# Kernel tuning notes

Measured on AMD Instinct MI355X. Metric: run time of the kernel, lower is better.

## Reference

```python
import jax, jax.numpy as jnp
import numpy as np

B, S, D, H = 4, 1024, 1024, 16
DK = D // H


def _linear_params(key, scale):
    kw, kb = jax.random.split(key)
    W = jax.random.normal(kw, (D, D), dtype=jnp.float32) * scale
    b = jax.random.normal(kb, (D,), dtype=jnp.float32) * 0.01
    return W, b


def setup_inputs() -> dict:
    key = jax.random.key(0)
    ks = jax.random.split(key, 12)
    scale = 1.0 / np.sqrt(D)
    inp = {
        "query": jax.random.normal(ks[0], (B, S, D), dtype=jnp.float32),
        "key": jax.random.normal(ks[1], (B, S, D), dtype=jnp.float32),
        "value": jax.random.normal(ks[2], (B, S, D), dtype=jnp.float32),
        "time_k": jax.random.normal(ks[3], (B, S, D), dtype=jnp.float32),
        "time_v": jax.random.normal(ks[4], (B, S, D), dtype=jnp.float32),
        "mask": jnp.zeros((B, 1, S, S), dtype=jnp.float32),
    }
    names = ["Wq", "bq", "Wk", "bk", "Wv", "bv", "Wtk", "btk", "Wtv", "btv", "Wm", "bm"]
    for i in range(6):
        W, b = _linear_params(ks[5 + i], scale)
        inp[names[2 * i]] = W
        inp[names[2 * i + 1]] = b
    return inp


def _split_heads(x):
    # [B,S,D] -> [B,H,S,DK]
    b, s, _ = x.shape
    return x.reshape(b, s, H, DK).transpose(0, 2, 1, 3)


def reference(query, key, value, time_k, time_v, mask,
              Wq, bq, Wk, bk, Wv, bv, Wtk, btk, Wtv, btv, Wm, bm):
    q = _split_heads(query @ Wq + bq)
    k = _split_heads(key @ Wk + bk)
    v = _split_heads(value @ Wv + bv)
    t_k = _split_heads(time_k @ Wtk + btk)
    t_v = _split_heads(time_v @ Wtv + btv)

    # scores[b,h,i,j] = q_i . k_j + t_k_i . q_j  (note second term uses q on the key axis)
    scores = jnp.einsum("bhid,bhjd->bhij", q, k) + jnp.einsum("bhid,bhjd->bhij", t_k, q)
    # module divides by sqrt(d_model) (query.size(-1)), not sqrt(d_k)
    scores = scores / jnp.sqrt(jnp.float32(D)) + mask
    probs = jax.nn.softmax(scores, axis=-1)

    # dropout is identity (p=0 / eval); squeeze(-2) is a no-op for S>1
    context = jnp.einsum("bhij,bhjd->bhid", probs, v) + jnp.einsum("bhij,bhjd->bhid", probs, t_v)
    x = context.transpose(0, 2, 1, 3).reshape(query.shape[0], -1, D)
    return x @ Wm + bm
```

## Files before the change

### kernel.cpp

```cpp
#include <hip/hip_runtime.h>
#include <hip/hip_bf16.h>
#include <cstdint>
#include <cstddef>

typedef __bf16 bf16;
typedef bf16 bf16x8 __attribute__((ext_vector_type(8)));
typedef bf16 bf16x4 __attribute__((ext_vector_type(4)));
typedef float f32x4 __attribute__((ext_vector_type(4)));
typedef unsigned int u32;

#define DEV static __device__ __forceinline__

DEV f32x4 mfma16(bf16x8 a, bf16x8 b, f32x4 c) {
    return __builtin_amdgcn_mfma_f32_16x16x32_bf16(a, b, c, 0, 0, 0);
}

DEV f32x4 shflx4(f32x4 v, int m) {
    f32x4 r;
    for (int i = 0; i < 4; ++i) r[i] = __shfl_xor(v[i], m, 64);
    return r;
}

DEV bf16x8 cvt8(const float* p) {
    float4 f0 = *(const float4*)p;
    float4 f1 = *(const float4*)(p + 4);
    bf16x8 v;
    v[0] = (bf16)f0.x; v[1] = (bf16)f0.y; v[2] = (bf16)f0.z; v[3] = (bf16)f0.w;
    v[4] = (bf16)f1.x; v[5] = (bf16)f1.y; v[6] = (bf16)f1.z; v[7] = (bf16)f1.w;
    return v;
}

DEV void glo(const bf16* g, bf16* l) {
    __builtin_amdgcn_global_load_lds(
        (const __attribute__((address_space(1))) u32*)g,
        (__attribute__((address_space(3))) u32*)l,
        16, 0, 0);
}

struct PrepArgs {
    const float* w[6];
    const float* act[5];
    bf16* wt;
    bf16* actbf[5];
};

__global__ __launch_bounds__(256) void prep_kernel(PrepArgs p)
{
    const int z = blockIdx.z;
    const int t = threadIdx.x;
    if (z < 6) {
        __shared__ bf16 tile[64][72];
        const float* src = p.w[z];
        bf16* out = p.wt + (size_t)z * 1024 * 1024;
        const int r = t >> 3, c8 = (t & 7) * 8;
        const int row0 = blockIdx.y * 64, col0 = blockIdx.x * 64;
        *(bf16x8*)&tile[r][c8]      = cvt8(&src[(size_t)(row0 + r) * 1024 + col0 + c8]);
        *(bf16x8*)&tile[r + 32][c8] = cvt8(&src[(size_t)(row0 + r + 32) * 1024 + col0 + c8]);
        __syncthreads();
        for (int half = 0; half < 2; ++half) {
            int rr = r + half * 32;
            bf16x8 v;
            for (int j = 0; j < 8; ++j) v[j] = tile[c8 + j][rr];
            *(bf16x8*)&out[(size_t)(col0 + rr) * 1024 + row0 + c8] = v;
        }
    } else {
        const float* src = p.act[z - 6];
        bf16* dst = p.actbf[z - 6];
        const size_t chunk = (size_t)(blockIdx.y * 16 + blockIdx.x) * 16384;
        for (int c = 0; c < 8; ++c) {
            const size_t off = chunk + (size_t)c * 2048 + (size_t)t * 8;
            *(bf16x8*)&dst[off] = cvt8(&src[off]);
        }
    }
}

__global__ __launch_bounds__(256) void maskprep_kernel(
    const float* __restrict__ mask, bf16* __restrict__ maskR)
{
    const int jt = blockIdx.x, it = blockIdx.y, b = blockIdx.z;
    __shared__ bf16 Mt[128 * 72];
    const int t = threadIdx.x, lane = t & 63, w = t >> 6;
    const int ln = lane & 15, qd = lane >> 4;
    {
        const int il = t >> 1, jh = (t & 1) * 32;
        const float* src = &mask[((size_t)b * 1024 + it * 128 + il) * 1024 + jt * 64 + jh];
        *(bf16x8*)&Mt[il * 72 + jh]      = cvt8(src);
        *(bf16x8*)&Mt[il * 72 + jh + 8]  = cvt8(src + 8);
        *(bf16x8*)&Mt[il * 72 + jh + 16] = cvt8(src + 16);
        *(bf16x8*)&Mt[il * 72 + jh + 24] = cvt8(src + 24);
    }
    __syncthreads();
    bf16 m[32];
    for (int si = 0; si < 2; ++si)
        for (int jc = 0; jc < 4; ++jc)
            for (int r = 0; r < 4; ++r) {
                const int il = w * 32 + si * 16 + qd * 4 + r;
                const int jl = jc * 16 + ln;
                m[(si * 4 + jc) * 4 + r] = Mt[il * 72 + jl];
            }
    bf16* dst = &maskR[((((size_t)b * 8 + it) * 16 + jt) * 256 + t) * 32];
    for (int c = 0; c < 4; ++c)
        *(bf16x8*)&dst[c * 8] = *(const bf16x8*)&m[c * 8];
}

struct ProjArgs {
    const bf16* A[5];
    const bf16* W[5];
    const float* bias[5];
    bf16* out[5];
    int vst[5];
};

#define WAITB(n) asm volatile("s_waitcnt vmcnt(" #n ")\n\ts_barrier" ::: "memory")

__global__ __launch_bounds__(256) void proj_gemm(ProjArgs pa)
{
    const int z = blockIdx.z;
    const bf16* A = pa.A[z];
    const bf16* W = pa.W[z];
    const int m0 = blockIdx.x * 128, n0 = blockIdx.y * 128;
    __shared__ bf16 As[4 * 128 * 32];
    __shared__ bf16 Bs[4 * 128 * 32];
    const int t = threadIdx.x, lane = t & 63, w = t >> 6;
    const int ln = lane & 15, qd = lane >> 4;
    const int wm0 = (w >> 1) * 64, wn0 = (w & 1) * 64;
    const int srow16 = lane >> 2;
    const int sseg   = lane & 3;

    f32x4 acc[4][4];
    for (int i = 0; i < 4; ++i)
        for (int j = 0; j < 4; ++j)
            acc[i][j] = (f32x4){0.f, 0.f, 0.f, 0.f};

#define STAGE_TILE(tt_) do {                                                   \
        const int _tt = (tt_);                                                 \
        const int _b = _tt & 3;                                                \
        const int _bk = _tt * 32;                                              \
        for (int _r = 0; _r < 2; ++_r) {                                       \
            const int _rows0 = _r * 64 + w * 16;                               \
            const int _row = _rows0 + srow16;                                  \
            const int _cs = (sseg ^ ((_row >> 1) & 3)) * 8;                    \
            glo(&A[(size_t)(m0 + _row) * 1024 + _bk + _cs],                    \
                &As[_b * 4096 + _rows0 * 32]);                                 \
            glo(&W[(size_t)(n0 + _row) * 1024 + _bk + _cs],                    \
                &Bs[_b * 4096 + _rows0 * 32]);                                 \
        }                                                                      \
    } while (0)

#define COMPUTE_TILE(tt_) do {                                                 \
        const int _b = (tt_) & 3;                                              \
        bf16x8 _af[4], _bf[4];                                                 \
        for (int _mi = 0; _mi < 4; ++_mi) {                                    \
            const int _row = wm0 + _mi * 16 + ln;                              \
            _af[_mi] = *(const bf16x8*)&As[_b * 4096 + _row * 32 +             \
                                           ((qd ^ ((_row >> 1) & 3)) * 8)];    \
        }                                                                      \
        for (int _ni = 0; _ni < 4; ++_ni) {                                    \
            const int _row = wn0 + _ni * 16 + ln;                              \
            _bf[_ni] = *(const bf16x8*)&Bs[_b * 4096 + _row * 32 +             \
                                           ((qd ^ ((_row >> 1) & 3)) * 8)];    \
        }                                                                      \
        __builtin_amdgcn_s_setprio(1);                                         \
        for (int _mi = 0; _mi < 4; ++_mi)                                      \
            for (int _ni = 0; _ni < 4; ++_ni)                                  \
                acc[_mi][_ni] = mfma16(_af[_mi], _bf[_ni], acc[_mi][_ni]);     \
        __builtin_amdgcn_s_setprio(0);                                         \
    } while (0)

    STAGE_TILE(0);
    STAGE_TILE(1);
    STAGE_TILE(2);
    WAITB(8);

    for (int tt = 0; tt < 29; ++tt) {
        STAGE_TILE(tt + 3);
        COMPUTE_TILE(tt);
        WAITB(8);
    }
    COMPUTE_TILE(29);
    WAITB(4);
    COMPUTE_TILE(30);
    WAITB(0);
    COMPUTE_TILE(31);

#undef STAGE_TILE
#undef COMPUTE_TILE

    const float* bias = pa.bias[z];
    bf16* out = pa.out[z];
    const int vst = pa.vst[z];
    for (int ni = 0; ni < 4; ++ni) {
        const int n = n0 + wn0 + ni * 16 + ln;
        const float bv = bias[n];
        for (int mi = 0; mi < 4; ++mi) {
            const int mbase = m0 + wm0 + mi * 16 + qd * 4;
            f32x4 v = acc[mi][ni];
            if (vst) {
                const int b = mbase >> 10, s = mbase & 1023;
                bf16x4 pk;
                for (int r = 0; r < 4; ++r) pk[r] = (bf16)(v[r] + bv);
                *(bf16x4*)&out[((size_t)(b * 1024 + n)) * 1024 + s] = pk;
            } else {
                for (int r = 0; r < 4; ++r)
                    out[(size_t)(mbase + r) * 1024 + n] = (bf16)(v[r] + bv);
            }
        }
    }
}

__global__ __launch_bounds__(256) void attn6_kernel(
    const bf16* __restrict__ Qb, const bf16* __restrict__ Kb, const bf16* __restrict__ TKb,
    const bf16* __restrict__ Va, const bf16* __restrict__ Vb,
    const bf16* __restrict__ maskR, bf16* __restrict__ ctx)
{
    const int h = blockIdx.x, it = blockIdx.y, b = blockIdx.z;
    const int i0 = it * 128;
    __shared__ bf16 Ks[64 * 64];
    __shared__ bf16 QJs[64 * 64];
    __shared__ bf16 Vs[64 * 68];
    __shared__ bf16 Ps[128][68];
    const int t = threadIdx.x, lane = t & 63, w = t >> 6;
    const int ln = lane & 15, qd = lane >> 4;
    const int lx = ln & 7;
    const size_t baseQ = ((size_t)b * 1024) * 1024 + (size_t)h * 64;

    bf16x8 qf[2][2], tkf[2][2];
    for (int si = 0; si < 2; ++si) {
        const size_t row = (size_t)(i0 + w * 32 + si * 16 + ln);
        for (int kc = 0; kc < 2; ++kc) {
            qf[si][kc]  = *(const bf16x8*)&Qb [baseQ + row * 1024 + kc * 32 + qd * 8];
            tkf[si][kc] = *(const bf16x8*)&TKb[baseQ + row * 1024 + kc * 32 + qd * 8];
        }
    }

    f32x4 O[2][4];
    f32x4 psum[2];
    for (int si = 0; si < 2; ++si) {
        psum[si] = (f32x4){0.f, 0.f, 0.f, 0.f};
        for (int dc = 0; dc < 4; ++dc) O[si][dc] = (f32x4){0.f, 0.f, 0.f, 0.f};
    }

    const float c1 = 0.045084439f;
    const float c2 = 1.442695041f;

    const size_t mtile0 = (((size_t)b * 8 + it) * 16) * 256 + t;

    for (int jt = 0; jt < 16; ++jt) {
        const int j0 = jt * 64;
        __syncthreads();
        {
            const int rr = lane >> 3;
            const int cbs = ((lane & 7) ^ rr) * 8;
            for (int i = 0; i < 4; ++i) {
                const int u = w * 4 + i;
                if (u < 8) {
                    glo(&Kb[baseQ + (size_t)(j0 + u * 8 + rr) * 1024 + cbs], &Ks[u * 512]);
                } else {
                    const int s = u - 8;
                    glo(&Qb[baseQ + (size_t)(j0 + s * 8 + rr) * 1024 + cbs], &QJs[s * 512]);
                }
            }
        }
        {
            const int vrow = t >> 2, vcol = (t & 3) * 16;
            const size_t va = ((size_t)b * 1024 + h * 64 + vrow) * 1024 + j0 + vcol;
            bf16x8 a0 = *(const bf16x8*)&Va[va];
            bf16x8 a1 = *(const bf16x8*)&Va[va + 8];
            bf16x8 b0 = *(const bf16x8*)&Vb[va];
            bf16x8 b1 = *(const bf16x8*)&Vb[va + 8];
            bf16 s[16];
            for (int e = 0; e < 8; ++e) {
                s[e]     = (bf16)((float)a0[e] + (float)b0[e]);
                s[8 + e] = (bf16)((float)a1[e] + (float)b1[e]);
            }
            bf16* dst = &Vs[vrow * 68 + vcol];
            for (int c = 0; c < 4; ++c)
                *(bf16x4*)&dst[c * 4] = *(const bf16x4*)&s[c * 4];
        }
        bf16x8 mm[4];
        {
            const bf16* mb = &maskR[(mtile0 + (size_t)jt * 256) * 32];
            for (int c = 0; c < 4; ++c) mm[c] = *(const bf16x8*)&mb[c * 8];
        }
        __syncthreads();

        f32x4 sc[2][4];
        for (int jc = 0; jc < 4; ++jc) {
            bf16x8 kf[2], qjf[2];
            for (int kc = 0; kc < 2; ++kc) {
                const int sg = ((kc * 4 + qd) ^ lx) * 8;
                kf[kc]  = *(const bf16x8*)&Ks [(jc * 16 + ln) * 64 + sg];
                qjf[kc] = *(const bf16x8*)&QJs[(jc * 16 + ln) * 64 + sg];
            }
            for (int si = 0; si < 2; ++si) {
                f32x4 a = (f32x4){0.f, 0.f, 0.f, 0.f};
                a = mfma16(qf[si][0], kf[0], a);
                a = mfma16(qf[si][1], kf[1], a);
                a = mfma16(tkf[si][0], qjf[0], a);
                a = mfma16(tkf[si][1], qjf[1], a);
                sc[si][jc] = a;
            }
        }
        for (int si = 0; si < 2; ++si) {
            const int ibl = w * 32 + si * 16 + qd * 4;
            for (int jc = 0; jc < 4; ++jc) {
                const int jl = jc * 16 + ln;
                const int e = si * 4 + jc;
                for (int r = 0; r < 4; ++r) {
                    const float mval = (float)mm[e >> 1][(e & 1) * 4 + r];
                    const float p = exp2f(fmaf(sc[si][jc][r], c1, mval * c2));
                    psum[si][r] += p;
                    Ps[ibl + r][jl] = (bf16)p;
                }
            }
        }
        for (int kc = 0; kc < 2; ++kc) {
            bf16x8 pa[2], vb[4];
            for (int si = 0; si < 2; ++si) {
                bf16x4 lo = *(const bf16x4*)&Ps[w * 32 + si * 16 + ln][kc * 32 + qd * 8];
                bf16x4 hi = *(const bf16x4*)&Ps[w * 32 + si * 16 + ln][kc * 32 + qd * 8 + 4];
                for (int e = 0; e < 4; ++e) { pa[si][e] = lo[e]; pa[si][4 + e] = hi[e]; }
            }
            for (int dc = 0; dc < 4; ++dc) {
                bf16x4 lo = *(const bf16x4*)&Vs[(dc * 16 + ln) * 68 + kc * 32 + qd * 8];
                bf16x4 hi = *(const bf16x4*)&Vs[(dc * 16 + ln) * 68 + kc * 32 + qd * 8 + 4];
                for (int e = 0; e < 4; ++e) { vb[dc][e] = lo[e]; vb[dc][4 + e] = hi[e]; }
            }
            for (int si = 0; si < 2; ++si)
                for (int dc = 0; dc < 4; ++dc)
                    O[si][dc] = mfma16(pa[si], vb[dc], O[si][dc]);
        }
    }

    for (int si = 0; si < 2; ++si) {
        for (int m = 1; m <= 8; m <<= 1) psum[si] += shflx4(psum[si], m);
        f32x4 rl;
        for (int r = 0; r < 4; ++r) rl[r] = 1.0f / psum[si][r];
        const int ibase = i0 + w * 32 + si * 16 + qd * 4;
        for (int dc = 0; dc < 4; ++dc) {
            const int d = h * 64 + dc * 16 + ln;
            f32x4 v = O[si][dc] * rl;
            for (int r = 0; r < 4; ++r)
                ctx[((size_t)b * 1024 + ibase + r) * 1024 + d] = (bf16)v[r];
        }
    }
}

__global__ __launch_bounds__(256) void out_gemm(
    const bf16* __restrict__ A, const bf16* __restrict__ W,
    const float* __restrict__ bias, float* __restrict__ out)
{
    const int m0 = blockIdx.x * 64, n0 = blockIdx.y * 128;
    __shared__ bf16 As[64 * 64];
    __shared__ bf16 Bs[128 * 64];
    const int t = threadIdx.x, lane = t & 63, w = t >> 6;
    const int ln = lane & 15, qd = lane >> 4;
    const int wn0 = w * 32;
    const int rr = lane >> 3;
    const int cbs = ((lane & 7) ^ rr) * 8;
    const int lx = ln & 7;
    f32x4 acc[4][2];
    for (int i = 0; i < 4; ++i)
        for (int j = 0; j < 2; ++j)
            acc[i][j] = (f32x4){0.f, 0.f, 0.f, 0.f};
    for (int ks = 0; ks < 16; ++ks) {
        const int bk = ks * 64;
        __syncthreads();
        for (int i = 0; i < 6; ++i) {
            const int u = w * 6 + i;
            if (u < 8) {
                glo(&A[(size_t)(m0 + u * 8 + rr) * 1024 + bk + cbs], &As[u * 512]);
            } else {
                const int sub = u - 8;
                glo(&W[(size_t)(n0 + sub * 8 + rr) * 1024 + bk + cbs], &Bs[sub * 512]);
            }
        }
        __syncthreads();
        for (int kc = 0; kc < 2; ++kc) {
            const int sg = ((kc * 4 + qd) ^ lx) * 8;
            bf16x8 af[4], bfr[2];
            for (int mi = 0; mi < 4; ++mi)
                af[mi] = *(const bf16x8*)&As[(mi * 16 + ln) * 64 + sg];
            for (int ni = 0; ni < 2; ++ni)
                bfr[ni] = *(const bf16x8*)&Bs[(wn0 + ni * 16 + ln) * 64 + sg];
            for (int mi = 0; mi < 4; ++mi)
                for (int ni = 0; ni < 2; ++ni)
                    acc[mi][ni] = mfma16(af[mi], bfr[ni], acc[mi][ni]);
        }
    }
    for (int ni = 0; ni < 2; ++ni) {
        const int n = n0 + wn0 + ni * 16 + ln;
        const float bv = bias[n];
        for (int mi = 0; mi < 4; ++mi) {
            const int mbase = m0 + mi * 16 + qd * 4;
            f32x4 v = acc[mi][ni];
            for (int r = 0; r < 4; ++r)
                out[(size_t)(mbase + r) * 1024 + n] = v[r] + bv;
        }
    }
}

extern "C" void kernel_launch(void* const* d_in, const int* in_sizes, int n_in,
                              void* d_out, int out_size, void* d_ws, size_t ws_size,
                              hipStream_t stream)
{
    (void)in_sizes; (void)n_in; (void)out_size; (void)ws_size;
    const float* query  = (const float*)d_in[0];
    const float* key    = (const float*)d_in[1];
    const float* value  = (const float*)d_in[2];
    const float* time_k = (const float*)d_in[3];
    const float* time_v = (const float*)d_in[4];
    const float* mask   = (const float*)d_in[5];
    const float* Wq  = (const float*)d_in[6];  const float* bq  = (const float*)d_in[7];
    const float* Wk  = (const float*)d_in[8];  const float* bk  = (const float*)d_in[9];
    const float* Wv  = (const float*)d_in[10]; const float* bv  = (const float*)d_in[11];
    const float* Wtk = (const float*)d_in[12]; const float* btk = (const float*)d_in[13];
    const float* Wtv = (const float*)d_in[14]; const float* btv = (const float*)d_in[15];
    const float* Wm  = (const float*)d_in[16]; const float* bm  = (const float*)d_in[17];

    bf16* ws = (bf16*)d_ws;
    const size_t MM = (size_t)1024 * 1024;
    bf16* WT    = ws;
    bf16* qbf   = ws + 6 * MM;
    bf16* kbf   = ws + 10 * MM;
    bf16* vbf   = ws + 14 * MM;
    bf16* tkbf  = ws + 18 * MM;
    bf16* tvbf  = ws + 22 * MM;
    bf16* Qb    = ws + 26 * MM;
    bf16* Kb    = ws + 30 * MM;
    bf16* TKb   = ws + 34 * MM;
    bf16* VsTa  = ws + 38 * MM;
    bf16* VsTb  = ws + 42 * MM;
    bf16* ctx   = ws + 6 * MM;
    bf16* maskR = (bf16*)d_out;

    PrepArgs pp;
    pp.w[0] = Wq; pp.w[1] = Wk; pp.w[2] = Wv; pp.w[3] = Wtk; pp.w[4] = Wtv; pp.w[5] = Wm;
    pp.wt = WT;
    pp.act[0] = query; pp.act[1] = key; pp.act[2] = value;
    pp.act[3] = time_k; pp.act[4] = time_v;
    pp.actbf[0] = qbf; pp.actbf[1] = kbf; pp.actbf[2] = vbf;
    pp.actbf[3] = tkbf; pp.actbf[4] = tvbf;
    prep_kernel<<<dim3(16, 16, 11), 256, 0, stream>>>(pp);
    maskprep_kernel<<<dim3(16, 8, 4), 256, 0, stream>>>(mask, maskR);

    ProjArgs pa;
    pa.A[0] = qbf;  pa.W[0] = WT + 0 * MM; pa.bias[0] = bq;  pa.out[0] = Qb;   pa.vst[0] = 0;
    pa.A[1] = kbf;  pa.W[1] = WT + 1 * MM; pa.bias[1] = bk;  pa.out[1] = Kb;   pa.vst[1] = 0;
    pa.A[2] = tkbf; pa.W[2] = WT + 3 * MM; pa.bias[2] = btk; pa.out[2] = TKb;  pa.vst[2] = 0;
    pa.A[3] = vbf;  pa.W[3] = WT + 2 * MM; pa.bias[3] = bv;  pa.out[3] = VsTa; pa.vst[3] = 1;
    pa.A[4] = tvbf; pa.W[4] = WT + 4 * MM; pa.bias[4] = btv; pa.out[4] = VsTb; pa.vst[4] = 1;
    proj_gemm<<<dim3(32, 8, 5), 256, 0, stream>>>(pa);

    attn6_kernel<<<dim3(16, 8, 4), 256, 0, stream>>>(
        Qb, Kb, TKb, VsTa, VsTb, maskR, ctx);
    out_gemm<<<dim3(64, 8), 256, 0, stream>>>(ctx, WT + 5 * MM, bm, (float*)d_out);
}
```

Before: 331.8 us.

## Enlarge projection GEMM tiles to 256x256 with 512 threads and shallower prefetch

The projection GEMM moves from 128x128 tiles with 4 waves to 256x256 tiles with 8 waves, each wave computing a 128x64 sub-tile. The global-load pipeline drops from three tiles in flight to two. The aim is to raise arithmetic intensity and operand reuse from LDS and global memory. In exchange, the grid shrinks to 320 blocks and LDS use grows to 128KB per block, which cuts occupancy and tail balance across CUs and leaves less latency hiding.

```diff
diff --git a/kernel.cpp b/kernel.cpp
--- a/kernel.cpp
+++ b/kernel.cpp
@@ -113,78 +113,73 @@
 
 #define WAITB(n) asm volatile("s_waitcnt vmcnt(" #n ")\n\ts_barrier" ::: "memory")
 
-__global__ __launch_bounds__(256) void proj_gemm(ProjArgs pa)
+__global__ __launch_bounds__(512, 2) void proj_gemm(ProjArgs pa)
 {
     const int z = blockIdx.z;
-    const bf16* A = pa.A[z];
-    const bf16* W = pa.W[z];
-    const int m0 = blockIdx.x * 128, n0 = blockIdx.y * 128;
-    __shared__ bf16 As[4 * 128 * 32];
-    __shared__ bf16 Bs[4 * 128 * 32];
+    const bf16* __restrict__ A = pa.A[z];
+    const bf16* __restrict__ W = pa.W[z];
+    const int m0 = blockIdx.x * 256, n0 = blockIdx.y * 256;
+    __shared__ bf16 As[4][256 * 32];
+    __shared__ bf16 Bs[4][256 * 32];
     const int t = threadIdx.x, lane = t & 63, w = t >> 6;
     const int ln = lane & 15, qd = lane >> 4;
-    const int wm0 = (w >> 1) * 64, wn0 = (w & 1) * 64;
-    const int srow16 = lane >> 2;
-    const int sseg   = lane & 3;
-
-    f32x4 acc[4][4];
-    for (int i = 0; i < 4; ++i)
+    const int wm0 = (w >> 2) * 128, wn0 = (w & 3) * 64;
+    const int srow = lane >> 2;
+    const int sseg = lane & 3;
+
+    f32x4 acc[8][4];
+    for (int i = 0; i < 8; ++i)
         for (int j = 0; j < 4; ++j)
             acc[i][j] = (f32x4){0.f, 0.f, 0.f, 0.f};
 
-#define STAGE_TILE(tt_) do {                                                   \
-        const int _tt = (tt_);                                                 \
-        const int _b = _tt & 3;                                                \
-        const int _bk = _tt * 32;                                              \
+#define STAGE(tt_) do {                                                        \
+        const int _b = (tt_) & 3;                                              \
+        const int _bk = (tt_) * 32;                                            \
         for (int _r = 0; _r < 2; ++_r) {                                       \
-            const int _rows0 = _r * 64 + w * 16;                               \
-            const int _row = _rows0 + srow16;                                  \
+            const int _row = _r * 128 + w * 16 + srow;                         \
             const int _cs = (sseg ^ ((_row >> 1) & 3)) * 8;                    \
             glo(&A[(size_t)(m0 + _row) * 1024 + _bk + _cs],                    \
-                &As[_b * 4096 + _rows0 * 32]);                                 \
+                &As[_b][(_r * 128 + w * 16) * 32]);                            \
             glo(&W[(size_t)(n0 + _row) * 1024 + _bk + _cs],                    \
-                &Bs[_b * 4096 + _rows0 * 32]);                                 \
+                &Bs[_b][(_r * 128 + w * 16) * 32]);                            \
         }                                                                      \
     } while (0)
 
-#define COMPUTE_TILE(tt_) do {                                                 \
+#define COMPUTE(tt_) do {                                                      \
         const int _b = (tt_) & 3;                                              \
-        bf16x8 _af[4], _bf[4];                                                 \
-        for (int _mi = 0; _mi < 4; ++_mi) {                                    \
+        bf16x8 _af[8], _bf[4];                                                 \
+        for (int _mi = 0; _mi < 8; ++_mi) {                                    \
             const int _row = wm0 + _mi * 16 + ln;                              \
-            _af[_mi] = *(const bf16x8*)&As[_b * 4096 + _row * 32 +             \
-                                           ((qd ^ ((_row >> 1) & 3)) * 8)];    \
+            _af[_mi] = *(const bf16x8*)&As[_b][_row * 32 +                     \
+                                              ((qd ^ ((_row >> 1) & 3)) * 8)]; \
         }                                                                      \
         for (int _ni = 0; _ni < 4; ++_ni) {                                    \
             const int _row = wn0 + _ni * 16 + ln;                              \
-            _bf[_ni] = *(const bf16x8*)&Bs[_b * 4096 + _row * 32 +             \
-                                           ((qd ^ ((_row >> 1) & 3)) * 8)];    \
+            _bf[_ni] = *(const bf16x8*)&Bs[_b][_row * 32 +                     \
+                                              ((qd ^ ((_row >> 1) & 3)) * 8)]; \
         }                                                                      \
         __builtin_amdgcn_s_setprio(1);                                         \
-        for (int _mi = 0; _mi < 4; ++_mi)                                      \
+        for (int _mi = 0; _mi < 8; ++_mi)                                      \
             for (int _ni = 0; _ni < 4; ++_ni)                                  \
                 acc[_mi][_ni] = mfma16(_af[_mi], _bf[_ni], acc[_mi][_ni]);     \
         __builtin_amdgcn_s_setprio(0);                                         \
     } while (0)
 
-    STAGE_TILE(0);
-    STAGE_TILE(1);
-    STAGE_TILE(2);
-    WAITB(8);
-
-    for (int tt = 0; tt < 29; ++tt) {
-        STAGE_TILE(tt + 3);
-        COMPUTE_TILE(tt);
-        WAITB(8);
-    }
-    COMPUTE_TILE(29);
+    STAGE(0);
+    STAGE(1);
     WAITB(4);
-    COMPUTE_TILE(30);
+
+    for (int tt = 0; tt < 30; ++tt) {
+        STAGE(tt + 2);
+        COMPUTE(tt);
+        WAITB(4);
+    }
+    COMPUTE(30);
     WAITB(0);
-    COMPUTE_TILE(31);
-
-#undef STAGE_TILE
-#undef COMPUTE_TILE
+    COMPUTE(31);
+
+#undef STAGE
+#undef COMPUTE
 
     const float* bias = pa.bias[z];
     bf16* out = pa.out[z];
@@ -192,7 +187,7 @@
     for (int ni = 0; ni < 4; ++ni) {
         const int n = n0 + wn0 + ni * 16 + ln;
         const float bv = bias[n];
-        for (int mi = 0; mi < 4; ++mi) {
+        for (int mi = 0; mi < 8; ++mi) {
             const int mbase = m0 + wm0 + mi * 16 + qd * 4;
             f32x4 v = acc[mi][ni];
             if (vst) {
@@ -450,7 +445,7 @@
     pa.A[2] = tkbf; pa.W[2] = WT + 3 * MM; pa.bias[2] = btk; pa.out[2] = TKb;  pa.vst[2] = 0;
     pa.A[3] = vbf;  pa.W[3] = WT + 2 * MM; pa.bias[3] = bv;  pa.out[3] = VsTa; pa.vst[3] = 1;
     pa.A[4] = tvbf; pa.W[4] = WT + 4 * MM; pa.bias[4] = btv; pa.out[4] = VsTb; pa.vst[4] = 1;
-    proj_gemm<<<dim3(32, 8, 5), 256, 0, stream>>>(pa);
+    proj_gemm<<<dim3(16, 4, 5), 512, 0, stream>>>(pa);
 
     attn6_kernel<<<dim3(16, 8, 4), 256, 0, stream>>>(
         Qb, Kb, TKb, VsTa, VsTb, maskR, ctx);
```

After: 344.4 us. +3.8%, slower.
